# Kernel tuning notes

Measured on AMD Instinct MI355X. Metric: run time of the kernel, lower is better.

Reference implementation:

```python
import jax, jax.numpy as jnp
import numpy as np

DIM = 2048
N_HEADS = 16
Q_LORA = 1536
KV_LORA = 512
NOPE = 128
ROPE = 64
QK_D = NOPE + ROPE  # 192
V_D = 128
EPS = 1e-6
B, S = 2, 2048


def rmsnorm(x, w, eps=EPS):
    return x * jax.lax.rsqrt(jnp.mean(x * x, axis=-1, keepdims=True) + eps) * w


def rotate_pe(x, cos, sin):
    # x: [B, S, H, ROPE]; cos/sin: [S, ROPE] -> broadcast [1, S, 1, ROPE]
    c = cos[None, :, None, :]
    s = sin[None, :, None, :]
    x1, x2 = jnp.split(x, 2, axis=-1)
    rot = jnp.concatenate([-x2, x1], axis=-1)
    return x * c + rot * s


def setup_inputs() -> dict:
    key = jax.random.key(0)
    ks = jax.random.split(key, 8)
    std = 0.02
    x = jax.random.normal(ks[0], (B, S, DIM), dtype=jnp.float32)
    # proper rotary tables
    inv_freq = 1.0 / (10000.0 ** (np.arange(0, ROPE, 2, dtype=np.float32) / ROPE))
    t = np.arange(S, dtype=np.float32)
    freqs = np.outer(t, inv_freq)  # [S, ROPE/2]
    emb = np.concatenate([freqs, freqs], axis=-1)  # [S, ROPE]
    cos = jnp.asarray(np.cos(emb))
    sin = jnp.asarray(np.sin(emb))
    wq_a = jax.random.normal(ks[1], (Q_LORA, DIM), dtype=jnp.float32) * std
    q_norm_w = jnp.ones((Q_LORA,), dtype=jnp.float32)
    wq_b = jax.random.normal(ks[2], (N_HEADS * QK_D, Q_LORA), dtype=jnp.float32) * std
    wkv_a = jax.random.normal(ks[3], (KV_LORA + ROPE, DIM), dtype=jnp.float32) * std
    kv_norm_w = jnp.ones((KV_LORA,), dtype=jnp.float32)
    wkv_b = jax.random.normal(ks[4], (N_HEADS * (NOPE + V_D), KV_LORA), dtype=jnp.float32) * std
    wo = jax.random.normal(ks[5], (DIM, N_HEADS * V_D), dtype=jnp.float32) * std
    return {"x": x, "cos": cos, "sin": sin, "wq_a": wq_a, "q_norm_w": q_norm_w,
            "wq_b": wq_b, "wkv_a": wkv_a, "kv_norm_w": kv_norm_w, "wkv_b": wkv_b, "wo": wo}


def mla_forward(x, cos, sin, wq_a, q_norm_w, wq_b, wkv_a, kv_norm_w, wkv_b, wo):
    bsz, seqlen, _ = x.shape
    scale = QK_D ** (-0.5)
    # Q path: low-rank down-proj -> RMSNorm -> up-proj
    q = rmsnorm(x @ wq_a.T, q_norm_w) @ wq_b.T
    q = q.reshape(bsz, seqlen, N_HEADS, QK_D)
    q_nope, q_pe = q[..., :NOPE], q[..., NOPE:]
    q_pe = rotate_pe(q_pe, cos, sin)
    q = jnp.concatenate([q_nope, q_pe], axis=-1)
    # KV path: shared low-rank latent + single rope slice
    kv = x @ wkv_a.T  # [B, S, KV_LORA + ROPE]
    kv_c, k_pe = kv[..., :KV_LORA], kv[..., KV_LORA:]
    k_pe = rotate_pe(k_pe[:, :, None, :], cos, sin)  # [B, S, 1, ROPE]
    kvb = rmsnorm(kv_c, kv_norm_w) @ wkv_b.T
    kvb = kvb.reshape(bsz, seqlen, N_HEADS, NOPE + V_D)
    k_nope, v = kvb[..., :NOPE], kvb[..., NOPE:]
    k = jnp.concatenate([k_nope, jnp.broadcast_to(k_pe, (bsz, seqlen, N_HEADS, ROPE))], axis=-1)
    # causal attention
    scores = jnp.einsum('bqhd,bkhd->bhqk', q, k) * scale
    mask = jnp.tril(jnp.ones((seqlen, seqlen), dtype=bool))
    scores = jnp.where(mask[None, None], scores, jnp.finfo(scores.dtype).min)
    p = jax.nn.softmax(scores, axis=-1)
    out = jnp.einsum('bhqk,bkhd->bqhd', p, v)
    out = out.reshape(bsz, seqlen, N_HEADS * V_D)
    return out @ wo.T


def reference(x, cos, sin, wq_a, q_norm_w, wq_b, wkv_a, kv_norm_w, wkv_b, wo):
    return mla_forward(x, cos, sin, wq_a, q_norm_w, wq_b, wkv_a, kv_norm_w, wkv_b, wo)
```

## Files before the change

### kernel.cpp

```cpp
#include <hip/hip_runtime.h>

typedef unsigned short u16;
typedef __attribute__((ext_vector_type(8))) short short8;
typedef __attribute__((ext_vector_type(4))) float floatx4;

__device__ __forceinline__ float bf2f(u16 u) {
  union { unsigned int i; float f; } v; v.i = ((unsigned int)u) << 16; return v.f;
}
__device__ __forceinline__ u16 f2bf(float f) {
  union { float f; unsigned int i; } v; v.f = f;
  unsigned int u = v.i;
  u += 0x7fffu + ((u >> 16) & 1u);
  return (u16)(u >> 16);
}

__device__ __forceinline__ void gld_lds16(const void* g, void* l) {
  __builtin_amdgcn_global_load_lds(
      (const __attribute__((address_space(1))) unsigned int*)g,
      (__attribute__((address_space(3))) unsigned int*)l, 16, 0, 0);
}

__global__ __launch_bounds__(256) void repack_all_k(
    const float* __restrict__ x, const float* __restrict__ wqa,
    const float* __restrict__ wkva, const float* __restrict__ wqb,
    const float* __restrict__ wkvb, const float* __restrict__ wo,
    u16* __restrict__ xb, u16* __restrict__ wcat, u16* __restrict__ wqbb,
    u16* __restrict__ wkbb, u16* __restrict__ wob) {
  long i = ((long)blockIdx.x * 256 + threadIdx.x) * 4;
  int region = blockIdx.y;
  const float* s = nullptr; u16* d = nullptr; long n = 0;
  switch (region) {
    case 0: s = x;    d = xb;   n = 4096L * 2048; break;
    case 1: s = nullptr; d = wcat; n = 2176L * 2048; break;
    case 2: s = wqb;  d = wqbb; n = 3072L * 1536; break;
    case 3: s = wkvb; d = wkbb; n = 4096L * 512;  break;
    case 4: s = wo;   d = wob;  n = 2048L * 2048; break;
  }
  if (i >= n) return;
  float4 v;
  if (region == 1) {
    long r = i >> 11, c = i & 2047;
    if (r < 1536)      v = *(const float4*)(wqa + r * 2048 + c);
    else if (r < 2112) v = *(const float4*)(wkva + (r - 1536) * 2048 + c);
    else               v = (float4){0.f, 0.f, 0.f, 0.f};
  } else {
    v = *(const float4*)(s + i);
  }
  d[i + 0] = f2bf(v.x); d[i + 1] = f2bf(v.y);
  d[i + 2] = f2bf(v.z); d[i + 3] = f2bf(v.w);
}

template <int OUT_F32>
__device__ __forceinline__ void gemm_tile(
    const u16* __restrict__ A, int lda, const u16* __restrict__ W, int ldw,
    void* __restrict__ Cv, int ldc, int K, int bm, int bn,
    u16* Asm, u16* Bsm) {
  int tid = threadIdx.x;
  int lane = tid & 63, w = tid >> 6;
  int wm = (w >> 1) * 64, wn = (w & 1) * 64;

  floatx4 acc[4][4];
#pragma unroll
  for (int i = 0; i < 4; i++)
#pragma unroll
    for (int j = 0; j < 4; j++) acc[i][j] = (floatx4){0.f, 0.f, 0.f, 0.f};

  int sr = lane >> 2;
  int sc = (lane & 3) * 8;
  int fr = lane & 15;
  int fq = (lane >> 4) * 8;

  for (int k0 = 0; k0 < K; k0 += 32) {
#pragma unroll
    for (int c = 0; c < 2; c++) {
      int row = 32 * w + 16 * c + sr;
      gld_lds16(A + (size_t)(bm + row) * lda + k0 + sc, &Asm[(32 * w + 16 * c) * 32]);
      gld_lds16(W + (size_t)(bn + row) * ldw + k0 + sc, &Bsm[(32 * w + 16 * c) * 32]);
    }
    __syncthreads();
    short8 af[4], bfr[4];
#pragma unroll
    for (int i = 0; i < 4; i++)
      af[i] = *(const short8*)&Asm[(wm + i * 16 + fr) * 32 + fq];
#pragma unroll
    for (int j = 0; j < 4; j++)
      bfr[j] = *(const short8*)&Bsm[(wn + j * 16 + fr) * 32 + fq];
#pragma unroll
    for (int i = 0; i < 4; i++)
#pragma unroll
      for (int j = 0; j < 4; j++)
        acc[i][j] = __builtin_amdgcn_mfma_f32_16x16x32_bf16(af[i], bfr[j], acc[i][j], 0, 0, 0);
    __syncthreads();
  }

  int cr = (lane >> 4) * 4, cc = lane & 15;
#pragma unroll
  for (int i = 0; i < 4; i++)
#pragma unroll
    for (int j = 0; j < 4; j++) {
      int col = bn + wn + j * 16 + cc;
#pragma unroll
      for (int r = 0; r < 4; r++) {
        size_t row = (size_t)(bm + wm + i * 16 + cr + r);
        if (OUT_F32) ((float*)Cv)[row * ldc + col] = acc[i][j][r];
        else         ((u16*)Cv)[row * ldc + col] = f2bf(acc[i][j][r]);
      }
    }
}

template <int OUT_F32>
__global__ __launch_bounds__(256) void gemm_bt_mfma(
    const u16* __restrict__ A, int lda,
    const u16* __restrict__ W, int ldw,
    void* __restrict__ Cv, int ldc, int K) {
  __shared__ u16 Asm[128 * 32];
  __shared__ u16 Bsm[128 * 32];
  gemm_tile<OUT_F32>(A, lda, W, ldw, Cv, ldc, K, blockIdx.y * 128, blockIdx.x * 128, Asm, Bsm);
}

__global__ __launch_bounds__(256) void gemm_dual_mfma(
    const u16* __restrict__ A1, int lda1, const u16* __restrict__ W1, int ldw1,
    u16* __restrict__ C1, int ldc1, int K1, int nt1,
    const u16* __restrict__ A2, int lda2, const u16* __restrict__ W2, int ldw2,
    u16* __restrict__ C2, int ldc2, int K2) {
  __shared__ u16 Asm[128 * 32];
  __shared__ u16 Bsm[128 * 32];
  int bx = blockIdx.x;
  if (bx < nt1)
    gemm_tile<0>(A1, lda1, W1, ldw1, C1, ldc1, K1, blockIdx.y * 128, bx * 128, Asm, Bsm);
  else
    gemm_tile<0>(A2, lda2, W2, ldw2, C2, ldc2, K2, blockIdx.y * 128, (bx - nt1) * 128, Asm, Bsm);
}

__global__ __launch_bounds__(256) void normrope_k(
    u16* __restrict__ qkv, const float* __restrict__ qnw,
    const float* __restrict__ kvnw, const float* __restrict__ cosb,
    const float* __restrict__ sinb, int S) {
  int row = blockIdx.x, tid = threadIdx.x;
  u16* p = qkv + (size_t)row * 2176;
  float s1 = 0.f, s2 = 0.f;
#pragma unroll
  for (int it = 0; it < 6; it++) { float v = bf2f(p[tid + 256 * it]); s1 += v * v; }
#pragma unroll
  for (int it = 0; it < 2; it++) { float v = bf2f(p[1536 + tid + 256 * it]); s2 += v * v; }
  for (int off = 32; off > 0; off >>= 1) {
    s1 += __shfl_down(s1, off);
    s2 += __shfl_down(s2, off);
  }
  __shared__ float red1[4], red2[4];
  if ((tid & 63) == 0) { red1[tid >> 6] = s1; red2[tid >> 6] = s2; }
  __syncthreads();
  float inv1 = rsqrtf((red1[0] + red1[1] + red1[2] + red1[3]) / 1536.f + 1e-6f);
  float inv2 = rsqrtf((red2[0] + red2[1] + red2[2] + red2[3]) / 512.f + 1e-6f);
#pragma unroll
  for (int it = 0; it < 6; it++) {
    int i = tid + 256 * it;
    p[i] = f2bf(bf2f(p[i]) * inv1 * qnw[i]);
  }
#pragma unroll
  for (int it = 0; it < 2; it++) {
    int i = tid + 256 * it;
    p[1536 + i] = f2bf(bf2f(p[1536 + i]) * inv2 * kvnw[i]);
  }
  if (tid < 32) {
    int pos = row % S;
    float c1 = cosb[pos * 64 + tid];
    float c2 = cosb[pos * 64 + tid + 32];
    float sn1 = sinb[pos * 64 + tid];
    float sn2 = sinb[pos * 64 + tid + 32];
    float x1 = bf2f(p[2048 + tid]), x2 = bf2f(p[2048 + tid + 32]);
    p[2048 + tid]      = f2bf(x1 * c1 - x2 * sn1);
    p[2048 + tid + 32] = f2bf(x2 * c2 + x1 * sn2);
  }
}

__global__ void rope_k(u16* __restrict__ base, int row_stride, int head_stride,
                       int head_off, const float* __restrict__ cosb,
                       const float* __restrict__ sinb, int S) {
  int t = blockIdx.x, h = blockIdx.y, i = threadIdx.x;
  int pos = t % S;
  u16* p = base + (size_t)t * row_stride + h * head_stride + head_off;
  float c1 = cosb[pos * 64 + i];
  float c2 = cosb[pos * 64 + i + 32];
  float s1 = sinb[pos * 64 + i];
  float s2 = sinb[pos * 64 + i + 32];
  float x1 = bf2f(p[i]), x2 = bf2f(p[i + 32]);
  p[i]      = f2bf(x1 * c1 - x2 * s1);
  p[i + 32] = f2bf(x2 * c2 + x1 * s2);
}

__global__ __launch_bounds__(256) void vtrans_k(
    const u16* __restrict__ kvb, u16* __restrict__ vt, int S) {
  int tb = blockIdx.x, h = blockIdx.y, b = blockIdx.z;
  __shared__ __align__(16) u16 Ts[64][136];
  int tid = threadIdx.x;
#pragma unroll
  for (int it = 0; it < 4; it++) {
    int e = tid + 256 * it;
    int tok = e >> 4, c = e & 15;
    short8 v = *(const short8*)(kvb + (size_t)(b * S + tb * 64 + tok) * 4096 + h * 256 + 128 + c * 8);
    *(short8*)&Ts[tok][c * 8] = v;
  }
  __syncthreads();
  int vd = tid >> 1, half = (tid & 1) * 32;
  u16 tmp[32];
#pragma unroll
  for (int j = 0; j < 32; j++) tmp[j] = Ts[half + j][vd];
  u16* dst = vt + ((size_t)((b * 16 + h) * 128) + vd) * S + tb * 64 + half;
#pragma unroll
  for (int c = 0; c < 4; c++)
    *(short8*)(dst + c * 8) = *(short8*)&tmp[c * 8];
}

#define AT_BK 64
__global__ __launch_bounds__(256) void attn_mfma(
    const u16* __restrict__ qf, const u16* __restrict__ kvb,
    const u16* __restrict__ kpe, int kpe_stride, const u16* __restrict__ vt,
    u16* __restrict__ at, int S) {
  int id = blockIdx.x;
  int pair = id >> 5, hb = id & 31;
  int h = hb & 15, b = hb >> 4;
  int NT = S / AT_BK;
  int tid = threadIdx.x, lane = tid & 63, w = tid >> 6;
  int fr = lane & 15, fq = lane >> 4;
  int fs = fr & 7;

  __shared__ __align__(16) u16 Ksn[AT_BK * 128];
  __shared__ __align__(16) u16 Ksp[AT_BK * 64];
  __shared__ __align__(16) u16 Vts[128 * AT_BK];
  __shared__ __align__(16) u16 Ps[64 * AT_BK];

  const float scale = 0.07216878364870323f;

  for (int p = 0; p < 2; p++) {
    int qt = p ? (NT - 1 - pair) : pair;
    int q0 = qt * 64;

    short8 qfrag[6];
    {
      const u16* qrow = qf + (size_t)(b * S + q0 + w * 16 + fr) * 3072 + h * 192 + fq * 8;
#pragma unroll
      for (int ks = 0; ks < 6; ks++) qfrag[ks] = *(const short8*)(qrow + ks * 32);
    }

    floatx4 acc_o[8];
#pragma unroll
    for (int j = 0; j < 8; j++) acc_o[j] = (floatx4){0.f, 0.f, 0.f, 0.f};
    float m_r[4], l_r[4];
#pragma unroll
    for (int r = 0; r < 4; r++) { m_r[r] = -3e38f; l_r[r] = 0.f; }

    for (int kt = 0; kt <= qt; kt++) {
      int k0 = kt * AT_BK;
      size_t tokbase = (size_t)(b * S + k0);
#pragma unroll
      for (int c = 0; c < 4; c++) {
        int row = w * 16 + c * 4 + (lane >> 4);
        int cg = (lane & 15) ^ (row & 7);
        gld_lds16(kvb + (tokbase + row) * 4096 + h * 256 + cg * 8,
                  &Ksn[(w * 16 + c * 4) * 128]);
      }
#pragma unroll
      for (int c = 0; c < 2; c++) {
        int row = w * 16 + c * 8 + (lane >> 3);
        int cg = (lane & 7) ^ (row & 7);
        gld_lds16(kpe + (tokbase + row) * kpe_stride + cg * 8,
                  &Ksp[(w * 16 + c * 8) * 64]);
      }
#pragma unroll
      for (int c = 0; c < 4; c++) {
        int vd = w * 32 + c * 8 + (lane >> 3);
        int cg = (lane & 7) ^ (vd & 7);
        gld_lds16(vt + ((size_t)((b * 16 + h) * 128) + vd) * S + k0 + cg * 8,
                  &Vts[(w * 32 + c * 8) * 64]);
      }
      __syncthreads();

      floatx4 accs[4];
#pragma unroll
      for (int nt = 0; nt < 4; nt++) accs[nt] = (floatx4){0.f, 0.f, 0.f, 0.f};
#pragma unroll
      for (int nt = 0; nt < 4; nt++) {
#pragma unroll
        for (int ks = 0; ks < 4; ks++) {
          short8 bf = *(const short8*)&Ksn[(nt * 16 + fr) * 128 + ((ks * 4 + fq) ^ fs) * 8];
          accs[nt] = __builtin_amdgcn_mfma_f32_16x16x32_bf16(qfrag[ks], bf, accs[nt], 0, 0, 0);
        }
#pragma unroll
        for (int ks = 0; ks < 2; ks++) {
          short8 bf = *(const short8*)&Ksp[(nt * 16 + fr) * 64 + ((ks * 4 + fq) ^ fs) * 8];
          accs[nt] = __builtin_amdgcn_mfma_f32_16x16x32_bf16(qfrag[4 + ks], bf, accs[nt], 0, 0, 0);
        }
      }

      bool diag = (kt == qt);
#pragma unroll
      for (int nt = 0; nt < 4; nt++)
#pragma unroll
        for (int r = 0; r < 4; r++) {
          float s = accs[nt][r] * scale;
          if (diag) {
            int col = nt * 16 + fr;
            int row = fq * 4 + r;
            if (k0 + col > q0 + w * 16 + row) s = -3e38f;
          }
          accs[nt][r] = s;
        }

      float alpha[4];
#pragma unroll
      for (int r = 0; r < 4; r++) {
        float mx = fmaxf(fmaxf(accs[0][r], accs[1][r]), fmaxf(accs[2][r], accs[3][r]));
        mx = fmaxf(mx, __shfl_xor(mx, 1));
        mx = fmaxf(mx, __shfl_xor(mx, 2));
        mx = fmaxf(mx, __shfl_xor(mx, 4));
        mx = fmaxf(mx, __shfl_xor(mx, 8));
        float mnew = fmaxf(m_r[r], mx);
        alpha[r] = __expf(m_r[r] - mnew);
        m_r[r] = mnew;
        l_r[r] *= alpha[r];
      }
#pragma unroll
      for (int nt = 0; nt < 4; nt++)
#pragma unroll
        for (int r = 0; r < 4; r++) {
          float pv = __expf(accs[nt][r] - m_r[r]);
          l_r[r] += pv;
          int row_p = w * 16 + fq * 4 + r;
          int col = nt * 16 + fr;
          Ps[row_p * 64 + (((col >> 3) ^ (row_p & 7)) * 8) + (col & 7)] = f2bf(pv);
        }
      __syncthreads();

#pragma unroll
      for (int j = 0; j < 8; j++)
#pragma unroll
        for (int r = 0; r < 4; r++) acc_o[j][r] *= alpha[r];
      short8 pf0 = *(const short8*)&Ps[(w * 16 + fr) * 64 + (fq ^ fs) * 8];
      short8 pf1 = *(const short8*)&Ps[(w * 16 + fr) * 64 + ((4 + fq) ^ fs) * 8];
#pragma unroll
      for (int j = 0; j < 8; j++) {
        short8 v0 = *(const short8*)&Vts[(j * 16 + fr) * 64 + (fq ^ fs) * 8];
        short8 v1 = *(const short8*)&Vts[(j * 16 + fr) * 64 + ((4 + fq) ^ fs) * 8];
        acc_o[j] = __builtin_amdgcn_mfma_f32_16x16x32_bf16(pf0, v0, acc_o[j], 0, 0, 0);
        acc_o[j] = __builtin_amdgcn_mfma_f32_16x16x32_bf16(pf1, v1, acc_o[j], 0, 0, 0);
      }
      __syncthreads();
    }

    float inv_l[4];
#pragma unroll
    for (int r = 0; r < 4; r++) {
      float sm = l_r[r];
      sm += __shfl_xor(sm, 1);
      sm += __shfl_xor(sm, 2);
      sm += __shfl_xor(sm, 4);
      sm += __shfl_xor(sm, 8);
      inv_l[r] = 1.f / sm;
    }
#pragma unroll
    for (int j = 0; j < 8; j++)
#pragma unroll
      for (int r = 0; r < 4; r++) {
        size_t row = (size_t)(b * S + q0 + w * 16 + fq * 4 + r);
        at[row * 2048 + h * 128 + j * 16 + fr] = f2bf(acc_o[j][r] * inv_l[r]);
      }
  }
}

extern "C" void kernel_launch(void* const* d_in, const int* in_sizes, int n_in,
                              void* d_out, int out_size, void* d_ws, size_t ws_size,
                              hipStream_t stream) {
  (void)in_sizes; (void)n_in; (void)out_size; (void)ws_size;
  const float* x     = (const float*)d_in[0];
  const float* cosb  = (const float*)d_in[1];
  const float* sinb  = (const float*)d_in[2];
  const float* wq_a  = (const float*)d_in[3];
  const float* qnw   = (const float*)d_in[4];
  const float* wq_b  = (const float*)d_in[5];
  const float* wkv_a = (const float*)d_in[6];
  const float* kvnw  = (const float*)d_in[7];
  const float* wkv_b = (const float*)d_in[8];
  const float* wo    = (const float*)d_in[9];
  float* out = (float*)d_out;
  const int B = 2, S = 2048, T = B * S;

  char* wsb = (char*)d_ws;
  size_t off = 0;
  u16* xb   = (u16*)(wsb + off); off += (size_t)T * 2048 * 2;
  u16* wcat = (u16*)(wsb + off); off += (size_t)2176 * 2048 * 2;
  u16* wqbb = (u16*)(wsb + off); off += (size_t)3072 * 1536 * 2;
  u16* wkbb = (u16*)(wsb + off); off += (size_t)4096 * 512 * 2;
  u16* wob  = (u16*)(wsb + off); off += (size_t)2048 * 2048 * 2;
  u16* qkv  = (u16*)(wsb + off); off += (size_t)T * 2176 * 2;
  u16* qf   = (u16*)(wsb + off); off += (size_t)T * 3072 * 2;
  u16* kvb  = (u16*)(wsb + off); off += (size_t)T * 4096 * 2;
  u16* at   = (u16*)(wsb + off); off += (size_t)T * 2048 * 2;
  u16* vt   = xb;

  repack_all_k<<<dim3(8192, 5), 256, 0, stream>>>(
      x, wq_a, wkv_a, wq_b, wkv_b, wo, xb, wcat, wqbb, wkbb, wob);

  gemm_bt_mfma<0><<<dim3(2176 / 128, T / 128), 256, 0, stream>>>(xb, 2048, wcat, 2048, qkv, 2176, 2048);
  normrope_k<<<T, 256, 0, stream>>>(qkv, qnw, kvnw, cosb, sinb, S);
  gemm_dual_mfma<<<dim3(3072 / 128 + 4096 / 128, T / 128), 256, 0, stream>>>(
      qkv, 2176, wqbb, 1536, qf, 3072, 1536, 3072 / 128,
      qkv + 1536, 2176, wkbb, 512, kvb, 4096, 512);
  rope_k<<<dim3(T, 16), 32, 0, stream>>>(qf, 3072, 192, 128, cosb, sinb, S);
  vtrans_k<<<dim3(S / 64, 16, B), 256, 0, stream>>>(kvb, vt, S);
  attn_mfma<<<dim3((S / 128) * 32), 256, 0, stream>>>(qf, kvb, qkv + 2048, 2176, vt, at, S);
  gemm_bt_mfma<1><<<dim3(2048 / 128, T / 128), 256, 0, stream>>>(at, 2048, wob, 2048, out, 2048, 2048);
}
```

Before: 487.2 us.

## Split attention into one q-tile per block, alias P buffer, add MFMA priority

Attention previously gave each block a pair of q-tiles (short and long). Now each block handles a single q-tile, which doubles the grid to 1024 blocks, and a four-segment ordering interleaves heavy and light tiles to balance load. The Ps buffer reuses the Ksp LDS region, made safe by an extra barrier after QK. This cuts LDS use and may raise occupancy. s_setprio wraps the MFMA loops, and rope_k is relaunched with 256-thread blocks covering 8 heads each to reduce tiny-block launch overhead.

```diff
diff --git a/kernel.cpp b/kernel.cpp
--- a/kernel.cpp
+++ b/kernel.cpp
@@ -174,10 +174,12 @@
   }
 }
 
-__global__ void rope_k(u16* __restrict__ base, int row_stride, int head_stride,
-                       int head_off, const float* __restrict__ cosb,
-                       const float* __restrict__ sinb, int S) {
-  int t = blockIdx.x, h = blockIdx.y, i = threadIdx.x;
+__global__ __launch_bounds__(256) void rope_k(
+    u16* __restrict__ base, int row_stride, int head_stride, int head_off,
+    const float* __restrict__ cosb, const float* __restrict__ sinb, int S) {
+  int t = blockIdx.x;
+  int h = blockIdx.y * 8 + (threadIdx.x >> 5);
+  int i = threadIdx.x & 31;
   int pos = t % S;
   u16* p = base + (size_t)t * row_stride + h * head_stride + head_off;
   float c1 = cosb[pos * 64 + i];
@@ -218,9 +220,17 @@
     const u16* __restrict__ kpe, int kpe_stride, const u16* __restrict__ vt,
     u16* __restrict__ at, int S) {
   int id = blockIdx.x;
-  int pair = id >> 5, hb = id & 31;
+  int NT = S / AT_BK;
+  int hb = id & 31;
   int h = hb & 15, b = hb >> 4;
-  int NT = S / AT_BK;
+  int j = id >> 5;
+  int q4 = NT >> 2;
+  int qt;
+  if (j < q4)            qt = NT - 1 - j;
+  else if (j < 2 * q4)   qt = j - q4;
+  else if (j < 3 * q4)   qt = 3 * q4 - 1 - (j - 2 * q4);
+  else                   qt = q4 + (j - 3 * q4);
+
   int tid = threadIdx.x, lane = tid & 63, w = tid >> 6;
   int fr = lane & 15, fq = lane >> 4;
   int fs = fr & 7;
@@ -228,144 +238,145 @@
   __shared__ __align__(16) u16 Ksn[AT_BK * 128];
   __shared__ __align__(16) u16 Ksp[AT_BK * 64];
   __shared__ __align__(16) u16 Vts[128 * AT_BK];
-  __shared__ __align__(16) u16 Ps[64 * AT_BK];
+  u16* Ps = Ksp;
 
   const float scale = 0.07216878364870323f;
-
-  for (int p = 0; p < 2; p++) {
-    int qt = p ? (NT - 1 - pair) : pair;
-    int q0 = qt * 64;
-
-    short8 qfrag[6];
-    {
-      const u16* qrow = qf + (size_t)(b * S + q0 + w * 16 + fr) * 3072 + h * 192 + fq * 8;
-#pragma unroll
-      for (int ks = 0; ks < 6; ks++) qfrag[ks] = *(const short8*)(qrow + ks * 32);
-    }
-
-    floatx4 acc_o[8];
-#pragma unroll
-    for (int j = 0; j < 8; j++) acc_o[j] = (floatx4){0.f, 0.f, 0.f, 0.f};
-    float m_r[4], l_r[4];
-#pragma unroll
-    for (int r = 0; r < 4; r++) { m_r[r] = -3e38f; l_r[r] = 0.f; }
-
-    for (int kt = 0; kt <= qt; kt++) {
-      int k0 = kt * AT_BK;
-      size_t tokbase = (size_t)(b * S + k0);
-#pragma unroll
-      for (int c = 0; c < 4; c++) {
-        int row = w * 16 + c * 4 + (lane >> 4);
-        int cg = (lane & 15) ^ (row & 7);
-        gld_lds16(kvb + (tokbase + row) * 4096 + h * 256 + cg * 8,
-                  &Ksn[(w * 16 + c * 4) * 128]);
+  int q0 = qt * 64;
+
+  short8 qfrag[6];
+  {
+    const u16* qrow = qf + (size_t)(b * S + q0 + w * 16 + fr) * 3072 + h * 192 + fq * 8;
+#pragma unroll
+    for (int ks = 0; ks < 6; ks++) qfrag[ks] = *(const short8*)(qrow + ks * 32);
+  }
+
+  floatx4 acc_o[8];
+#pragma unroll
+  for (int jj = 0; jj < 8; jj++) acc_o[jj] = (floatx4){0.f, 0.f, 0.f, 0.f};
+  float m_r[4], l_r[4];
+#pragma unroll
+  for (int r = 0; r < 4; r++) { m_r[r] = -3e38f; l_r[r] = 0.f; }
+
+  for (int kt = 0; kt <= qt; kt++) {
+    int k0 = kt * AT_BK;
+    size_t tokbase = (size_t)(b * S + k0);
+#pragma unroll
+    for (int c = 0; c < 4; c++) {
+      int row = w * 16 + c * 4 + (lane >> 4);
+      int cg = (lane & 15) ^ (row & 7);
+      gld_lds16(kvb + (tokbase + row) * 4096 + h * 256 + cg * 8,
+                &Ksn[(w * 16 + c * 4) * 128]);
+    }
+#pragma unroll
+    for (int c = 0; c < 2; c++) {
+      int row = w * 16 + c * 8 + (lane >> 3);
+      int cg = (lane & 7) ^ (row & 7);
+      gld_lds16(kpe + (tokbase + row) * kpe_stride + cg * 8,
+                &Ksp[(w * 16 + c * 8) * 64]);
+    }
+#pragma unroll
+    for (int c = 0; c < 4; c++) {
+      int vd = w * 32 + c * 8 + (lane >> 3);
+      int cg = (lane & 7) ^ (vd & 7);
+      gld_lds16(vt + ((size_t)((b * 16 + h) * 128) + vd) * S + k0 + cg * 8,
+                &Vts[(w * 32 + c * 8) * 64]);
+    }
+    __syncthreads();
+
+    floatx4 accs[4];
+#pragma unroll
+    for (int nt = 0; nt < 4; nt++) accs[nt] = (floatx4){0.f, 0.f, 0.f, 0.f};
+    __builtin_amdgcn_s_setprio(1);
+#pragma unroll
+    for (int nt = 0; nt < 4; nt++) {
+#pragma unroll
+      for (int ks = 0; ks < 4; ks++) {
+        short8 bf = *(const short8*)&Ksn[(nt * 16 + fr) * 128 + ((ks * 4 + fq) ^ fs) * 8];
+        accs[nt] = __builtin_amdgcn_mfma_f32_16x16x32_bf16(qfrag[ks], bf, accs[nt], 0, 0, 0);
       }
 #pragma unroll
-      for (int c = 0; c < 2; c++) {
-        int row = w * 16 + c * 8 + (lane >> 3);
-        int cg = (lane & 7) ^ (row & 7);
-        gld_lds16(kpe + (tokbase + row) * kpe_stride + cg * 8,
-                  &Ksp[(w * 16 + c * 8) * 64]);
+      for (int ks = 0; ks < 2; ks++) {
+        short8 bf = *(const short8*)&Ksp[(nt * 16 + fr) * 64 + ((ks * 4 + fq) ^ fs) * 8];
+        accs[nt] = __builtin_amdgcn_mfma_f32_16x16x32_bf16(qfrag[4 + ks], bf, accs[nt], 0, 0, 0);
       }
-#pragma unroll
-      for (int c = 0; c < 4; c++) {
-        int vd = w * 32 + c * 8 + (lane >> 3);
-        int cg = (lane & 7) ^ (vd & 7);
-        gld_lds16(vt + ((size_t)((b * 16 + h) * 128) + vd) * S + k0 + cg * 8,
-                  &Vts[(w * 32 + c * 8) * 64]);
+    }
+    __builtin_amdgcn_s_setprio(0);
+    __syncthreads();
+
+    bool diag = (kt == qt);
+#pragma unroll
+    for (int nt = 0; nt < 4; nt++)
+#pragma unroll
+      for (int r = 0; r < 4; r++) {
+        float s = accs[nt][r] * scale;
+        if (diag) {
+          int col = nt * 16 + fr;
+          int row = fq * 4 + r;
+          if (k0 + col > q0 + w * 16 + row) s = -3e38f;
+        }
+        accs[nt][r] = s;
       }
-      __syncthreads();
-
-      floatx4 accs[4];
-#pragma unroll
-      for (int nt = 0; nt < 4; nt++) accs[nt] = (floatx4){0.f, 0.f, 0.f, 0.f};
-#pragma unroll
-      for (int nt = 0; nt < 4; nt++) {
-#pragma unroll
-        for (int ks = 0; ks < 4; ks++) {
-          short8 bf = *(const short8*)&Ksn[(nt * 16 + fr) * 128 + ((ks * 4 + fq) ^ fs) * 8];
-          accs[nt] = __builtin_amdgcn_mfma_f32_16x16x32_bf16(qfrag[ks], bf, accs[nt], 0, 0, 0);
-        }
-#pragma unroll
-        for (int ks = 0; ks < 2; ks++) {
-          short8 bf = *(const short8*)&Ksp[(nt * 16 + fr) * 64 + ((ks * 4 + fq) ^ fs) * 8];
-          accs[nt] = __builtin_amdgcn_mfma_f32_16x16x32_bf16(qfrag[4 + ks], bf, accs[nt], 0, 0, 0);
-        }
+
+    float alpha[4];
+#pragma unroll
+    for (int r = 0; r < 4; r++) {
+      float mx = fmaxf(fmaxf(accs[0][r], accs[1][r]), fmaxf(accs[2][r], accs[3][r]));
+      mx = fmaxf(mx, __shfl_xor(mx, 1));
+      mx = fmaxf(mx, __shfl_xor(mx, 2));
+      mx = fmaxf(mx, __shfl_xor(mx, 4));
+      mx = fmaxf(mx, __shfl_xor(mx, 8));
+      float mnew = fmaxf(m_r[r], mx);
+      alpha[r] = __expf(m_r[r] - mnew);
+      m_r[r] = mnew;
+      l_r[r] *= alpha[r];
+    }
+#pragma unroll
+    for (int nt = 0; nt < 4; nt++)
+#pragma unroll
+      for (int r = 0; r < 4; r++) {
+        float pv = __expf(accs[nt][r] - m_r[r]);
+        l_r[r] += pv;
+        int row_p = w * 16 + fq * 4 + r;
+        int col = nt * 16 + fr;
+        Ps[row_p * 64 + (((col >> 3) ^ (row_p & 7)) * 8) + (col & 7)] = f2bf(pv);
       }
-
-      bool diag = (kt == qt);
-#pragma unroll
-      for (int nt = 0; nt < 4; nt++)
-#pragma unroll
-        for (int r = 0; r < 4; r++) {
-          float s = accs[nt][r] * scale;
-          if (diag) {
-            int col = nt * 16 + fr;
-            int row = fq * 4 + r;
-            if (k0 + col > q0 + w * 16 + row) s = -3e38f;
-          }
-          accs[nt][r] = s;
-        }
-
-      float alpha[4];
-#pragma unroll
-      for (int r = 0; r < 4; r++) {
-        float mx = fmaxf(fmaxf(accs[0][r], accs[1][r]), fmaxf(accs[2][r], accs[3][r]));
-        mx = fmaxf(mx, __shfl_xor(mx, 1));
-        mx = fmaxf(mx, __shfl_xor(mx, 2));
-        mx = fmaxf(mx, __shfl_xor(mx, 4));
-        mx = fmaxf(mx, __shfl_xor(mx, 8));
-        float mnew = fmaxf(m_r[r], mx);
-        alpha[r] = __expf(m_r[r] - mnew);
-        m_r[r] = mnew;
-        l_r[r] *= alpha[r];
-      }
-#pragma unroll
-      for (int nt = 0; nt < 4; nt++)
-#pragma unroll
-        for (int r = 0; r < 4; r++) {
-          float pv = __expf(accs[nt][r] - m_r[r]);
-          l_r[r] += pv;
-          int row_p = w * 16 + fq * 4 + r;
-          int col = nt * 16 + fr;
-          Ps[row_p * 64 + (((col >> 3) ^ (row_p & 7)) * 8) + (col & 7)] = f2bf(pv);
-        }
-      __syncthreads();
-
-#pragma unroll
-      for (int j = 0; j < 8; j++)
-#pragma unroll
-        for (int r = 0; r < 4; r++) acc_o[j][r] *= alpha[r];
-      short8 pf0 = *(const short8*)&Ps[(w * 16 + fr) * 64 + (fq ^ fs) * 8];
-      short8 pf1 = *(const short8*)&Ps[(w * 16 + fr) * 64 + ((4 + fq) ^ fs) * 8];
-#pragma unroll
-      for (int j = 0; j < 8; j++) {
-        short8 v0 = *(const short8*)&Vts[(j * 16 + fr) * 64 + (fq ^ fs) * 8];
-        short8 v1 = *(const short8*)&Vts[(j * 16 + fr) * 64 + ((4 + fq) ^ fs) * 8];
-        acc_o[j] = __builtin_amdgcn_mfma_f32_16x16x32_bf16(pf0, v0, acc_o[j], 0, 0, 0);
-        acc_o[j] = __builtin_amdgcn_mfma_f32_16x16x32_bf16(pf1, v1, acc_o[j], 0, 0, 0);
-      }
-      __syncthreads();
-    }
-
-    float inv_l[4];
+    __syncthreads();
+
+#pragma unroll
+    for (int jj = 0; jj < 8; jj++)
+#pragma unroll
+      for (int r = 0; r < 4; r++) acc_o[jj][r] *= alpha[r];
+    short8 pf0 = *(const short8*)&Ps[(w * 16 + fr) * 64 + (fq ^ fs) * 8];
+    short8 pf1 = *(const short8*)&Ps[(w * 16 + fr) * 64 + ((4 + fq) ^ fs) * 8];
+    __builtin_amdgcn_s_setprio(1);
+#pragma unroll
+    for (int jj = 0; jj < 8; jj++) {
+      short8 v0 = *(const short8*)&Vts[(jj * 16 + fr) * 64 + (fq ^ fs) * 8];
+      short8 v1 = *(const short8*)&Vts[(jj * 16 + fr) * 64 + ((4 + fq) ^ fs) * 8];
+      acc_o[jj] = __builtin_amdgcn_mfma_f32_16x16x32_bf16(pf0, v0, acc_o[jj], 0, 0, 0);
+      acc_o[jj] = __builtin_amdgcn_mfma_f32_16x16x32_bf16(pf1, v1, acc_o[jj], 0, 0, 0);
+    }
+    __builtin_amdgcn_s_setprio(0);
+    __syncthreads();
+  }
+
+  float inv_l[4];
+#pragma unroll
+  for (int r = 0; r < 4; r++) {
+    float sm = l_r[r];
+    sm += __shfl_xor(sm, 1);
+    sm += __shfl_xor(sm, 2);
+    sm += __shfl_xor(sm, 4);
+    sm += __shfl_xor(sm, 8);
+    inv_l[r] = 1.f / sm;
+  }
+#pragma unroll
+  for (int jj = 0; jj < 8; jj++)
 #pragma unroll
     for (int r = 0; r < 4; r++) {
-      float sm = l_r[r];
-      sm += __shfl_xor(sm, 1);
-      sm += __shfl_xor(sm, 2);
-      sm += __shfl_xor(sm, 4);
-      sm += __shfl_xor(sm, 8);
-      inv_l[r] = 1.f / sm;
-    }
-#pragma unroll
-    for (int j = 0; j < 8; j++)
-#pragma unroll
-      for (int r = 0; r < 4; r++) {
-        size_t row = (size_t)(b * S + q0 + w * 16 + fq * 4 + r);
-        at[row * 2048 + h * 128 + j * 16 + fr] = f2bf(acc_o[j][r] * inv_l[r]);
-      }
-  }
+      size_t row = (size_t)(b * S + q0 + w * 16 + fq * 4 + r);
+      at[row * 2048 + h * 128 + jj * 16 + fr] = f2bf(acc_o[jj][r] * inv_l[r]);
+    }
 }
 
 extern "C" void kernel_launch(void* const* d_in, const int* in_sizes, int n_in,
@@ -406,8 +417,8 @@
   gemm_dual_mfma<<<dim3(3072 / 128 + 4096 / 128, T / 128), 256, 0, stream>>>(
       qkv, 2176, wqbb, 1536, qf, 3072, 1536, 3072 / 128,
       qkv + 1536, 2176, wkbb, 512, kvb, 4096, 512);
-  rope_k<<<dim3(T, 16), 32, 0, stream>>>(qf, 3072, 192, 128, cosb, sinb, S);
+  rope_k<<<dim3(T, 2), 256, 0, stream>>>(qf, 3072, 192, 128, cosb, sinb, S);
   vtrans_k<<<dim3(S / 64, 16, B), 256, 0, stream>>>(kvb, vt, S);
-  attn_mfma<<<dim3((S / 128) * 32), 256, 0, stream>>>(qf, kvb, qkv + 2048, 2176, vt, at, S);
+  attn_mfma<<<dim3((S / AT_BK) * 32), 256, 0, stream>>>(qf, kvb, qkv + 2048, 2176, vt, at, S);
   gemm_bt_mfma<1><<<dim3(2048 / 128, T / 128), 256, 0, stream>>>(at, 2048, wob, 2048, out, 2048, 2048);
 }
```

After: 485.8 us. No clear change (-0.3%).
